# Kernel tuning notes

Hardware: AMD Instinct MI355X
Metric: run time of the kernel (lower is better)

## Reference

```python
import jax, jax.numpy as jnp
import numpy as np

EPS = 1e-8  # torch CosineSimilarity default eps


def setup_inputs() -> dict:
    key = jax.random.key(0)
    k_emb, k_ei, k_w1, k_w2, k_b1, k_b2 = jax.random.split(key, 6)
    N, H, E = 50000, 256, 300000
    emb = jax.random.normal(k_emb, (N, H), dtype=jnp.float32)
    edge_index = jax.random.randint(k_ei, (2, E), 0, N, dtype=jnp.int64)
    # Xavier-uniform init for the two Linear layers (fan_in = fan_out = H)
    limit = float(np.sqrt(6.0 / (H + H)))
    W1 = jax.random.uniform(k_w1, (H, H), minval=-limit, maxval=limit, dtype=jnp.float32)
    W2 = jax.random.uniform(k_w2, (H, H), minval=-limit, maxval=limit, dtype=jnp.float32)
    b1 = jnp.zeros((H,), dtype=jnp.float32)
    b2 = jnp.zeros((H,), dtype=jnp.float32)
    return {"emb": emb, "edge_index": edge_index, "W1": W1, "b1": b1, "W2": W2, "b2": b2}


def _mlp(x, W1, b1, W2, b2):
    # Linear -> Dropout(eval: identity) -> ReLU -> Linear
    h = jax.nn.relu(x @ W1.T + b1)
    return h @ W2.T + b2


def _cosine(a, b):
    # torch.nn.CosineSimilarity(dim=1): dot / (max(||a||, eps) * max(||b||, eps))
    dot = jnp.sum(a * b, axis=1)
    na = jnp.maximum(jnp.linalg.norm(a, axis=1), EPS)
    nb = jnp.maximum(jnp.linalg.norm(b, axis=1), EPS)
    return dot / (na * nb)


def reference(emb, edge_index, W1, b1, W2, b2):
    col, row = edge_index[0], edge_index[1]
    f1 = emb[col]  # [E, H]
    f2 = emb[row]  # [E, H]
    g1 = _mlp(f1, W1, b1, W2, b2)
    g2 = _mlp(f2, W1, b1, W2, b2)
    return _cosine(g1, g2)  # [E] per-edge attention logits
```

## Files before the change

### kernel.cpp

```cpp
#include <hip/hip_runtime.h>
#include <stdint.h>

#define H 256
#define EPS 1e-8f

typedef __bf16 bf16x8 __attribute__((ext_vector_type(8)));
typedef float  f32x4  __attribute__((ext_vector_type(4)));

__device__ __forceinline__ unsigned short f2bf(float f) {
  unsigned u = __builtin_bit_cast(unsigned, f);
  u += 0x7FFFu + ((u >> 16) & 1u);
  return (unsigned short)(u >> 16);
}
__device__ __forceinline__ float bflo(unsigned u){ return __builtin_bit_cast(float, u << 16); }
__device__ __forceinline__ float bfhi(unsigned u){ return __builtin_bit_cast(float, u & 0xFFFF0000u); }

__device__ __forceinline__ void g2l16(const void* g, void* l) {
  __builtin_amdgcn_global_load_lds((__attribute__((address_space(1))) void*)g,
                                   (__attribute__((address_space(3))) void*)l, 16, 0, 0);
}

__global__ __launch_bounds__(256) void conv_bf16_kernel(
    const float* __restrict__ src, unsigned short* __restrict__ dst, int valid, int total) {
  int i = (blockIdx.x * 256 + threadIdx.x) * 4;
  if (i >= total) return;
  float4 v = make_float4(0.f, 0.f, 0.f, 0.f);
  if (i < valid) v = *(const float4*)(src + i);
  ushort4 o;
  o.x = f2bf(v.x); o.y = f2bf(v.y); o.z = f2bf(v.z); o.w = f2bf(v.w);
  *(ushort4*)(dst + i) = o;
}

__global__ __launch_bounds__(256) void conv_w_kernel(
    const float* __restrict__ W1, const float* __restrict__ W2,
    unsigned short* __restrict__ w1B, unsigned short* __restrict__ w2B) {
  int i = (blockIdx.x * 256 + threadIdx.x) * 4;
  const int HH = H * H;
  if (i >= 2 * HH) return;
  const float* s = (i < HH) ? W1 : W2;
  unsigned short* d = (i < HH) ? w1B : w2B;
  int j = (i < HH) ? i : i - HH;
  float4 v = *(const float4*)(s + j);
  ushort4 o;
  o.x = f2bf(v.x); o.y = f2bf(v.y); o.z = f2bf(v.z); o.w = f2bf(v.w);
  *(ushort4*)(d + j) = o;
}

__global__ __launch_bounds__(256) void fused_mlp_kernel(
    const unsigned short* __restrict__ A,
    const unsigned short* __restrict__ W1,
    const unsigned short* __restrict__ W2,
    const float* __restrict__ b1, const float* __restrict__ b2,
    unsigned short* __restrict__ G,
    float* __restrict__ rn) {
  __shared__ unsigned short sA[64 * 32];
  __shared__ unsigned short sW[256 * 32];
  __shared__ unsigned short sW2[256 * 32];
  __shared__ unsigned short sH[64 * 256];
  __shared__ float ssb[64][2];

  const int tid  = threadIdx.x;
  const int wave = tid >> 6, lane = tid & 63;
  const int quad = lane >> 4, l16 = lane & 15;
  const int wr = wave >> 1, wn = wave & 1;
  const size_t bm = blockIdx.x;

  const int arow = tid >> 2, kch = (tid & 3) * 8;
  const unsigned short* gA  = A  + ((bm * 64 + arow) * H + kch);
  const unsigned short* gW1 = W1 + (size_t)arow * H + kch;
  const unsigned short* gW2 = W2 + (size_t)arow * H + kch;
  unsigned short* lA  = sA  + tid * 8;
  unsigned short* lW  = sW  + tid * 8;
  unsigned short* lW2 = sW2 + tid * 8;

  f32x4 acc[8][2];
#pragma unroll
  for (int i = 0; i < 8; i++)
#pragma unroll
    for (int j = 0; j < 2; j++) acc[i][j] = (f32x4){0.f, 0.f, 0.f, 0.f};

#pragma unroll
  for (int ks = 0; ks < 8; ++ks) {
    const int k0 = ks * 32;
    if (ks) __syncthreads();
    g2l16(gA + k0, lA);
#pragma unroll
    for (int c = 0; c < 4; c++)
      g2l16(gW1 + (size_t)(c * 64) * H + k0, lW + c * 2048);
    __syncthreads();

    bf16x8 wf[8], af[2];
#pragma unroll
    for (int i = 0; i < 8; i++)
      wf[i] = *(const bf16x8*)(sW + ((wn * 128 + i * 16 + l16) * 32 + quad * 8));
#pragma unroll
    for (int j = 0; j < 2; j++)
      af[j] = *(const bf16x8*)(sA + ((wr * 32 + j * 16 + l16) * 32 + quad * 8));
#pragma unroll
    for (int i = 0; i < 8; i++)
#pragma unroll
      for (int j = 0; j < 2; j++)
        acc[i][j] = __builtin_amdgcn_mfma_f32_16x16x32_bf16(wf[i], af[j], acc[i][j], 0, 0, 0);
  }

#pragma unroll
  for (int c = 0; c < 4; c++)
    g2l16(gW2 + (size_t)(c * 64) * H, lW2 + c * 2048);

#pragma unroll
  for (int i = 0; i < 8; i++) {
    const int hcol = wn * 128 + i * 16 + quad * 4;
    const float4 bv = *(const float4*)(b1 + hcol);
#pragma unroll
    for (int j = 0; j < 2; j++) {
      const int row = wr * 32 + j * 16 + l16;
      f32x4 v = acc[i][j];
      unsigned short h0 = f2bf(fmaxf(v[0] + bv.x, 0.f));
      unsigned short h1 = f2bf(fmaxf(v[1] + bv.y, 0.f));
      unsigned short h2 = f2bf(fmaxf(v[2] + bv.z, 0.f));
      unsigned short h3 = f2bf(fmaxf(v[3] + bv.w, 0.f));
      uint2 p;
      p.x = (unsigned)h0 | ((unsigned)h1 << 16);
      p.y = (unsigned)h2 | ((unsigned)h3 << 16);
      unsigned off = (unsigned)(row * 512 + hcol * 2) ^ ((unsigned)(row & 7) << 4);
      *(uint2*)((char*)sH + off) = p;
    }
  }

  __syncthreads();

  f32x4 acc2[2][8];
#pragma unroll
  for (int i = 0; i < 2; i++)
#pragma unroll
    for (int j = 0; j < 8; j++) acc2[i][j] = (f32x4){0.f, 0.f, 0.f, 0.f};

#pragma unroll
  for (int ks = 0; ks < 8; ++ks) {
    if (ks) {
      __syncthreads();
#pragma unroll
      for (int c = 0; c < 4; c++)
        g2l16(gW2 + (size_t)(c * 64) * H + ks * 32, lW2 + c * 2048);
      __syncthreads();
    }
    bf16x8 hf[2], wf2[8];
#pragma unroll
    for (int i = 0; i < 2; i++) {
      const int hrow = wr * 32 + i * 16 + l16;
      unsigned off = (unsigned)(hrow * 512 + ks * 64 + quad * 16) ^ ((unsigned)(hrow & 7) << 4);
      hf[i] = *(const bf16x8*)((const char*)sH + off);
    }
#pragma unroll
    for (int j = 0; j < 8; j++)
      wf2[j] = *(const bf16x8*)(sW2 + ((wn * 128 + j * 16 + l16) * 32 + quad * 8));
#pragma unroll
    for (int i = 0; i < 2; i++)
#pragma unroll
      for (int j = 0; j < 8; j++)
        acc2[i][j] = __builtin_amdgcn_mfma_f32_16x16x32_bf16(hf[i], wf2[j], acc2[i][j], 0, 0, 0);
  }

  float b2v[8];
#pragma unroll
  for (int j = 0; j < 8; j++) b2v[j] = b2[wn * 128 + j * 16 + l16];
#pragma unroll
  for (int i = 0; i < 2; i++)
#pragma unroll
    for (int j = 0; j < 8; j++)
#pragma unroll
      for (int r = 0; r < 4; r++) acc2[i][j][r] += b2v[j];

  float ss[2][4];
#pragma unroll
  for (int i = 0; i < 2; i++)
#pragma unroll
    for (int r = 0; r < 4; r++) {
      float s = 0.f;
#pragma unroll
      for (int j = 0; j < 8; j++) s += acc2[i][j][r] * acc2[i][j][r];
      ss[i][r] = s;
    }
#pragma unroll
  for (int m = 1; m < 16; m <<= 1)
#pragma unroll
    for (int i = 0; i < 2; i++)
#pragma unroll
      for (int r = 0; r < 4; r++) ss[i][r] += __shfl_xor(ss[i][r], m, 64);
  if (l16 == 0) {
#pragma unroll
    for (int i = 0; i < 2; i++)
#pragma unroll
      for (int r = 0; r < 4; r++) ssb[wr * 32 + i * 16 + quad * 4 + r][wn] = ss[i][r];
  }
  __syncthreads();
  if (tid < 64) {
    float s2 = ssb[tid][0] + ssb[tid][1];
    rn[bm * 64 + tid] = 1.f / fmaxf(sqrtf(s2), EPS);
  }

#pragma unroll
  for (int i = 0; i < 2; i++)
#pragma unroll
    for (int j = 0; j < 8; j++) {
      const int gcol = wn * 128 + j * 16 + l16;
#pragma unroll
      for (int r = 0; r < 4; r++) {
        const size_t grow = bm * 64 + wr * 32 + i * 16 + quad * 4 + r;
        G[grow * H + gcol] = f2bf(acc2[i][j][r]);
      }
    }
}

__device__ __forceinline__ float dot_u4(uint4 a, uint4 b) {
  float s;
  s  = bflo(a.x) * bflo(b.x) + bfhi(a.x) * bfhi(b.x);
  s += bflo(a.y) * bflo(b.y) + bfhi(a.y) * bfhi(b.y);
  s += bflo(a.z) * bflo(b.z) + bfhi(a.z) * bfhi(b.z);
  s += bflo(a.w) * bflo(b.w) + bfhi(a.w) * bfhi(b.w);
  return s;
}

__global__ __launch_bounds__(256) void edge_cos_kernel(
    const int* __restrict__ ei, const unsigned short* __restrict__ g,
    const float* __restrict__ rn, float* __restrict__ out, int E) {
  const int lane = threadIdx.x & 63;
  const int wid  = threadIdx.x >> 6;
  const int l8   = lane & 7;
  const int sub  = lane >> 3;
  const int e    = blockIdx.x * 32 + wid * 8 + sub;
  if (e >= E) return;
  const int c = ei[e], r = ei[E + e];
  const uint4* gc = (const uint4*)(g + (size_t)c * H);
  const uint4* gr = (const uint4*)(g + (size_t)r * H);
  uint4 a0 = gc[l8], a1 = gc[l8 + 8], a2 = gc[l8 + 16], a3 = gc[l8 + 24];
  uint4 b0 = gr[l8], b1 = gr[l8 + 8], b2 = gr[l8 + 16], b3 = gr[l8 + 24];
  float d = dot_u4(a0, b0) + dot_u4(a1, b1) + dot_u4(a2, b2) + dot_u4(a3, b3);
  d += __shfl_xor(d, 4, 8);
  d += __shfl_xor(d, 2, 8);
  d += __shfl_xor(d, 1, 8);
  if (l8 == 0) out[e] = d * rn[c] * rn[r];
}

extern "C" void kernel_launch(void* const* d_in, const int* in_sizes, int n_in,
                              void* d_out, int out_size, void* d_ws, size_t ws_size,
                              hipStream_t stream) {
  const float* emb = (const float*)d_in[0];
  const int*   ei  = (const int*)d_in[1];
  const float* W1  = (const float*)d_in[2];
  const float* b1  = (const float*)d_in[3];
  const float* W2  = (const float*)d_in[4];
  const float* b2  = (const float*)d_in[5];
  float* out = (float*)d_out;

  const int NH = in_sizes[0];
  const int N  = NH / H;
  const int E  = in_sizes[1] / 2;
  const int Mp = ((N + 63) / 64) * 64;

  char* ws = (char*)d_ws;
  unsigned short* embB = (unsigned short*)ws; ws += (size_t)Mp * H * 2;
  unsigned short* gB   = (unsigned short*)ws; ws += (size_t)Mp * H * 2;
  unsigned short* w1B  = (unsigned short*)ws; ws += (size_t)H * H * 2;
  unsigned short* w2B  = (unsigned short*)ws; ws += (size_t)H * H * 2;
  float* rn            = (float*)ws;

  conv_bf16_kernel<<<(Mp * H / 4 + 255) / 256, 256, 0, stream>>>(emb, embB, NH, Mp * H);
  conv_w_kernel<<<(2 * H * H / 4 + 255) / 256, 256, 0, stream>>>(W1, W2, w1B, w2B);

  fused_mlp_kernel<<<Mp / 64, 256, 0, stream>>>(embB, w1B, w2B, b1, b2, gB, rn);

  edge_cos_kernel<<<(E + 31) / 32, 256, 0, stream>>>(ei, gB, rn, out, E);
}
```

Measured before the change: 165.7 us.

## Fuse embedding bf16 conversion into MLP kernel and double-buffer weight staging

Removes the separate fp32-to-bf16 conversion pass over the embedding table. The MLP kernel now reads fp32 rows directly, keeping three k-tiles in flight in registers and converting them into a double-buffered LDS tile. Weight tiles for both GEMMs are also double-buffered, so each iteration prefetches the next tile with a single barrier instead of two. This saves a full write and re-read of the bf16 embedding copy and a kernel launch, at the cost of more registers and higher LDS pressure per block.

Result: faster. 155.3 us (-6.3%).

```diff
diff --git a/kernel.cpp b/kernel.cpp
--- a/kernel.cpp
+++ b/kernel.cpp
@@ -18,17 +18,6 @@
 __device__ __forceinline__ void g2l16(const void* g, void* l) {
   __builtin_amdgcn_global_load_lds((__attribute__((address_space(1))) void*)g,
                                    (__attribute__((address_space(3))) void*)l, 16, 0, 0);
-}
-
-__global__ __launch_bounds__(256) void conv_bf16_kernel(
-    const float* __restrict__ src, unsigned short* __restrict__ dst, int valid, int total) {
-  int i = (blockIdx.x * 256 + threadIdx.x) * 4;
-  if (i >= total) return;
-  float4 v = make_float4(0.f, 0.f, 0.f, 0.f);
-  if (i < valid) v = *(const float4*)(src + i);
-  ushort4 o;
-  o.x = f2bf(v.x); o.y = f2bf(v.y); o.z = f2bf(v.z); o.w = f2bf(v.w);
-  *(ushort4*)(dst + i) = o;
 }
 
 __global__ __launch_bounds__(256) void conv_w_kernel(
@@ -47,15 +36,14 @@
 }
 
 __global__ __launch_bounds__(256) void fused_mlp_kernel(
-    const unsigned short* __restrict__ A,
+    const float* __restrict__ Af,
     const unsigned short* __restrict__ W1,
     const unsigned short* __restrict__ W2,
     const float* __restrict__ b1, const float* __restrict__ b2,
     unsigned short* __restrict__ G,
-    float* __restrict__ rn) {
-  __shared__ unsigned short sA[64 * 32];
-  __shared__ unsigned short sW[256 * 32];
-  __shared__ unsigned short sW2[256 * 32];
+    float* __restrict__ rn, int N) {
+  __shared__ unsigned short sA[2][64 * 32];
+  __shared__ unsigned short sW[2][256 * 32];
   __shared__ unsigned short sH[64 * 256];
   __shared__ float ssb[64][2];
 
@@ -66,12 +54,38 @@
   const size_t bm = blockIdx.x;
 
   const int arow = tid >> 2, kch = (tid & 3) * 8;
-  const unsigned short* gA  = A  + ((bm * 64 + arow) * H + kch);
+  const int grow = (int)bm * 64 + arow;
+  const bool avalid = grow < N;
+  const float* gAf = Af + (size_t)grow * H + kch;
   const unsigned short* gW1 = W1 + (size_t)arow * H + kch;
   const unsigned short* gW2 = W2 + (size_t)arow * H + kch;
-  unsigned short* lA  = sA  + tid * 8;
-  unsigned short* lW  = sW  + tid * 8;
-  unsigned short* lW2 = sW2 + tid * 8;
+
+  float4 ra[3][2];
+#define LOAD_A(kt, slot)                                                        \
+  do {                                                                          \
+    if (avalid) {                                                               \
+      ra[slot][0] = *(const float4*)(gAf + (kt) * 32);                          \
+      ra[slot][1] = *(const float4*)(gAf + (kt) * 32 + 4);                      \
+    } else {                                                                    \
+      ra[slot][0] = make_float4(0.f, 0.f, 0.f, 0.f);                            \
+      ra[slot][1] = make_float4(0.f, 0.f, 0.f, 0.f);                            \
+    }                                                                           \
+  } while (0)
+#define WRITE_A(buf, slot)                                                      \
+  do {                                                                          \
+    uint4 p;                                                                    \
+    p.x = (unsigned)f2bf(ra[slot][0].x) | ((unsigned)f2bf(ra[slot][0].y) << 16);\
+    p.y = (unsigned)f2bf(ra[slot][0].z) | ((unsigned)f2bf(ra[slot][0].w) << 16);\
+    p.z = (unsigned)f2bf(ra[slot][1].x) | ((unsigned)f2bf(ra[slot][1].y) << 16);\
+    p.w = (unsigned)f2bf(ra[slot][1].z) | ((unsigned)f2bf(ra[slot][1].w) << 16);\
+    *(uint4*)(&sA[buf][tid * 8]) = p;                                           \
+  } while (0)
+#define STAGE_W(gW, kt, buf)                                                    \
+  do {                                                                          \
+    _Pragma("unroll")                                                           \
+    for (int c = 0; c < 4; c++)                                                 \
+      g2l16((gW) + (size_t)(c * 64) * H + (kt) * 32, &sW[buf][c * 2048 + tid * 8]); \
+  } while (0)
 
   f32x4 acc[8][2];
 #pragma unroll
@@ -79,33 +93,34 @@
 #pragma unroll
     for (int j = 0; j < 2; j++) acc[i][j] = (f32x4){0.f, 0.f, 0.f, 0.f};
 
-#pragma unroll
-  for (int ks = 0; ks < 8; ++ks) {
-    const int k0 = ks * 32;
-    if (ks) __syncthreads();
-    g2l16(gA + k0, lA);
-#pragma unroll
-    for (int c = 0; c < 4; c++)
-      g2l16(gW1 + (size_t)(c * 64) * H + k0, lW + c * 2048);
-    __syncthreads();
+  LOAD_A(0, 0); LOAD_A(1, 1); LOAD_A(2, 2);
+  WRITE_A(0, 0);
+  STAGE_W(gW1, 0, 0);
+  __syncthreads();
+
+#pragma unroll
+  for (int kt = 0; kt < 8; ++kt) {
+    if (kt < 5) LOAD_A(kt + 3, (kt + 3) % 3);
+    if (kt < 7) STAGE_W(gW1, kt + 1, (kt + 1) & 1);
+    if (kt == 7) STAGE_W(gW2, 0, 0);
 
     bf16x8 wf[8], af[2];
 #pragma unroll
     for (int i = 0; i < 8; i++)
-      wf[i] = *(const bf16x8*)(sW + ((wn * 128 + i * 16 + l16) * 32 + quad * 8));
+      wf[i] = *(const bf16x8*)(&sW[kt & 1][(wn * 128 + i * 16 + l16) * 32 + quad * 8]);
 #pragma unroll
     for (int j = 0; j < 2; j++)
-      af[j] = *(const bf16x8*)(sA + ((wr * 32 + j * 16 + l16) * 32 + quad * 8));
+      af[j] = *(const bf16x8*)(&sA[kt & 1][(wr * 32 + j * 16 + l16) * 32 + quad * 8]);
+
+    if (kt < 7) WRITE_A((kt + 1) & 1, (kt + 1) % 3);
+
 #pragma unroll
     for (int i = 0; i < 8; i++)
 #pragma unroll
       for (int j = 0; j < 2; j++)
         acc[i][j] = __builtin_amdgcn_mfma_f32_16x16x32_bf16(wf[i], af[j], acc[i][j], 0, 0, 0);
-  }
-
-#pragma unroll
-  for (int c = 0; c < 4; c++)
-    g2l16(gW2 + (size_t)(c * 64) * H, lW2 + c * 2048);
+    __syncthreads();
+  }
 
 #pragma unroll
   for (int i = 0; i < 8; i++) {
@@ -136,29 +151,25 @@
     for (int j = 0; j < 8; j++) acc2[i][j] = (f32x4){0.f, 0.f, 0.f, 0.f};
 
 #pragma unroll
-  for (int ks = 0; ks < 8; ++ks) {
-    if (ks) {
-      __syncthreads();
-#pragma unroll
-      for (int c = 0; c < 4; c++)
-        g2l16(gW2 + (size_t)(c * 64) * H + ks * 32, lW2 + c * 2048);
-      __syncthreads();
-    }
+  for (int kt = 0; kt < 8; ++kt) {
+    if (kt < 7) STAGE_W(gW2, kt + 1, (kt + 1) & 1);
+
     bf16x8 hf[2], wf2[8];
 #pragma unroll
     for (int i = 0; i < 2; i++) {
       const int hrow = wr * 32 + i * 16 + l16;
-      unsigned off = (unsigned)(hrow * 512 + ks * 64 + quad * 16) ^ ((unsigned)(hrow & 7) << 4);
+      unsigned off = (unsigned)(hrow * 512 + kt * 64 + quad * 16) ^ ((unsigned)(hrow & 7) << 4);
       hf[i] = *(const bf16x8*)((const char*)sH + off);
     }
 #pragma unroll
     for (int j = 0; j < 8; j++)
-      wf2[j] = *(const bf16x8*)(sW2 + ((wn * 128 + j * 16 + l16) * 32 + quad * 8));
+      wf2[j] = *(const bf16x8*)(&sW[kt & 1][(wn * 128 + j * 16 + l16) * 32 + quad * 8]);
 #pragma unroll
     for (int i = 0; i < 2; i++)
 #pragma unroll
       for (int j = 0; j < 8; j++)
         acc2[i][j] = __builtin_amdgcn_mfma_f32_16x16x32_bf16(hf[i], wf2[j], acc2[i][j], 0, 0, 0);
+    __syncthreads();
   }
 
   float b2v[8];
@@ -206,10 +217,13 @@
       const int gcol = wn * 128 + j * 16 + l16;
 #pragma unroll
       for (int r = 0; r < 4; r++) {
-        const size_t grow = bm * 64 + wr * 32 + i * 16 + quad * 4 + r;
-        G[grow * H + gcol] = f2bf(acc2[i][j][r]);
+        const size_t grow2 = bm * 64 + wr * 32 + i * 16 + quad * 4 + r;
+        G[grow2 * H + gcol] = f2bf(acc2[i][j][r]);
       }
     }
+#undef LOAD_A
+#undef WRITE_A
+#undef STAGE_W
 }
 
 __device__ __forceinline__ float dot_u4(uint4 a, uint4 b) {
@@ -259,16 +273,14 @@
   const int Mp = ((N + 63) / 64) * 64;
 
   char* ws = (char*)d_ws;
-  unsigned short* embB = (unsigned short*)ws; ws += (size_t)Mp * H * 2;
   unsigned short* gB   = (unsigned short*)ws; ws += (size_t)Mp * H * 2;
   unsigned short* w1B  = (unsigned short*)ws; ws += (size_t)H * H * 2;
   unsigned short* w2B  = (unsigned short*)ws; ws += (size_t)H * H * 2;
   float* rn            = (float*)ws;
 
-  conv_bf16_kernel<<<(Mp * H / 4 + 255) / 256, 256, 0, stream>>>(emb, embB, NH, Mp * H);
   conv_w_kernel<<<(2 * H * H / 4 + 255) / 256, 256, 0, stream>>>(W1, W2, w1B, w2B);
 
-  fused_mlp_kernel<<<Mp / 64, 256, 0, stream>>>(embB, w1B, w2B, b1, b2, gB, rn);
+  fused_mlp_kernel<<<Mp / 64, 256, 0, stream>>>(emb, w1B, w2B, b1, b2, gB, rn, N);
 
   edge_cos_kernel<<<(E + 31) / 32, 256, 0, stream>>>(ei, gB, rn, out, E);
 }
```

## Fuse fp32-to-bf16 embedding conversion into MLP kernel and load operands directly

Applied to the files above, without the earlier changes.

Removes the separate embedding conversion kernel and its bf16 workspace. The MLP kernel now reads fp32 embeddings directly into registers and packs them to bf16. W1 and W2 fragments are loaded straight from global memory (expected to hit L2) instead of being staged through LDS with barriers. This avoids a full write and re-read of the embedding table and drops most syncthreads. In exchange, weight loads are uncoalesced per-wave global reads and register pressure rises.

After: 240.8 us. 1.45x slower.

```diff
diff --git a/kernel.cpp b/kernel.cpp
--- a/kernel.cpp
+++ b/kernel.cpp
@@ -15,20 +15,13 @@
 __device__ __forceinline__ float bflo(unsigned u){ return __builtin_bit_cast(float, u << 16); }
 __device__ __forceinline__ float bfhi(unsigned u){ return __builtin_bit_cast(float, u & 0xFFFF0000u); }
 
-__device__ __forceinline__ void g2l16(const void* g, void* l) {
-  __builtin_amdgcn_global_load_lds((__attribute__((address_space(1))) void*)g,
-                                   (__attribute__((address_space(3))) void*)l, 16, 0, 0);
-}
-
-__global__ __launch_bounds__(256) void conv_bf16_kernel(
-    const float* __restrict__ src, unsigned short* __restrict__ dst, int valid, int total) {
-  int i = (blockIdx.x * 256 + threadIdx.x) * 4;
-  if (i >= total) return;
-  float4 v = make_float4(0.f, 0.f, 0.f, 0.f);
-  if (i < valid) v = *(const float4*)(src + i);
-  ushort4 o;
-  o.x = f2bf(v.x); o.y = f2bf(v.y); o.z = f2bf(v.z); o.w = f2bf(v.w);
-  *(ushort4*)(dst + i) = o;
+__device__ __forceinline__ bf16x8 pack8(float4 a, float4 b) {
+  uint4 p;
+  p.x = (unsigned)f2bf(a.x) | ((unsigned)f2bf(a.y) << 16);
+  p.y = (unsigned)f2bf(a.z) | ((unsigned)f2bf(a.w) << 16);
+  p.z = (unsigned)f2bf(b.x) | ((unsigned)f2bf(b.y) << 16);
+  p.w = (unsigned)f2bf(b.z) | ((unsigned)f2bf(b.w) << 16);
+  return __builtin_bit_cast(bf16x8, p);
 }
 
 __global__ __launch_bounds__(256) void conv_w_kernel(
@@ -47,15 +40,12 @@
 }
 
 __global__ __launch_bounds__(256) void fused_mlp_kernel(
-    const unsigned short* __restrict__ A,
+    const float* __restrict__ Af,
     const unsigned short* __restrict__ W1,
     const unsigned short* __restrict__ W2,
     const float* __restrict__ b1, const float* __restrict__ b2,
     unsigned short* __restrict__ G,
-    float* __restrict__ rn) {
-  __shared__ unsigned short sA[64 * 32];
-  __shared__ unsigned short sW[256 * 32];
-  __shared__ unsigned short sW2[256 * 32];
+    float* __restrict__ rn, int N) {
   __shared__ unsigned short sH[64 * 256];
   __shared__ float ssb[64][2];
 
@@ -65,13 +55,13 @@
   const int wr = wave >> 1, wn = wave & 1;
   const size_t bm = blockIdx.x;
 
-  const int arow = tid >> 2, kch = (tid & 3) * 8;
-  const unsigned short* gA  = A  + ((bm * 64 + arow) * H + kch);
-  const unsigned short* gW1 = W1 + (size_t)arow * H + kch;
-  const unsigned short* gW2 = W2 + (size_t)arow * H + kch;
-  unsigned short* lA  = sA  + tid * 8;
-  unsigned short* lW  = sW  + tid * 8;
-  unsigned short* lW2 = sW2 + tid * 8;
+  const int arow0 = (int)bm * 64 + wr * 32 + l16;
+  const int arow1 = arow0 + 16;
+  const bool v0 = arow0 < N, v1 = arow1 < N;
+  const float* pA0 = Af + (size_t)arow0 * H + quad * 8;
+  const float* pA1 = Af + (size_t)arow1 * H + quad * 8;
+  const unsigned short* pW1 = W1 + (size_t)(wn * 128 + l16) * H + quad * 8;
+  const unsigned short* pW2 = W2 + (size_t)(wn * 128 + l16) * H + quad * 8;
 
   f32x4 acc[8][2];
 #pragma unroll
@@ -79,33 +69,26 @@
 #pragma unroll
     for (int j = 0; j < 2; j++) acc[i][j] = (f32x4){0.f, 0.f, 0.f, 0.f};
 
-#pragma unroll
-  for (int ks = 0; ks < 8; ++ks) {
-    const int k0 = ks * 32;
-    if (ks) __syncthreads();
-    g2l16(gA + k0, lA);
-#pragma unroll
-    for (int c = 0; c < 4; c++)
-      g2l16(gW1 + (size_t)(c * 64) * H + k0, lW + c * 2048);
-    __syncthreads();
-
-    bf16x8 wf[8], af[2];
+  const float4 z4 = make_float4(0.f, 0.f, 0.f, 0.f);
+#pragma unroll
+  for (int kt = 0; kt < 8; ++kt) {
+    const int k0 = kt * 32;
+    bf16x8 wf[8];
 #pragma unroll
     for (int i = 0; i < 8; i++)
-      wf[i] = *(const bf16x8*)(sW + ((wn * 128 + i * 16 + l16) * 32 + quad * 8));
-#pragma unroll
-    for (int j = 0; j < 2; j++)
-      af[j] = *(const bf16x8*)(sA + ((wr * 32 + j * 16 + l16) * 32 + quad * 8));
-#pragma unroll
-    for (int i = 0; i < 8; i++)
-#pragma unroll
-      for (int j = 0; j < 2; j++)
-        acc[i][j] = __builtin_amdgcn_mfma_f32_16x16x32_bf16(wf[i], af[j], acc[i][j], 0, 0, 0);
-  }
-
-#pragma unroll
-  for (int c = 0; c < 4; c++)
-    g2l16(gW2 + (size_t)(c * 64) * H, lW2 + c * 2048);
+      wf[i] = *(const bf16x8*)(pW1 + (size_t)(i * 16) * H + k0);
+    float4 a00 = v0 ? *(const float4*)(pA0 + k0)     : z4;
+    float4 a01 = v0 ? *(const float4*)(pA0 + k0 + 4) : z4;
+    float4 a10 = v1 ? *(const float4*)(pA1 + k0)     : z4;
+    float4 a11 = v1 ? *(const float4*)(pA1 + k0 + 4) : z4;
+    bf16x8 af0 = pack8(a00, a01);
+    bf16x8 af1 = pack8(a10, a11);
+#pragma unroll
+    for (int i = 0; i < 8; i++) {
+      acc[i][0] = __builtin_amdgcn_mfma_f32_16x16x32_bf16(wf[i], af0, acc[i][0], 0, 0, 0);
+      acc[i][1] = __builtin_amdgcn_mfma_f32_16x16x32_bf16(wf[i], af1, acc[i][1], 0, 0, 0);
+    }
+  }
 
 #pragma unroll
   for (int i = 0; i < 8; i++) {
@@ -136,24 +119,18 @@
     for (int j = 0; j < 8; j++) acc2[i][j] = (f32x4){0.f, 0.f, 0.f, 0.f};
 
 #pragma unroll
-  for (int ks = 0; ks < 8; ++ks) {
-    if (ks) {
-      __syncthreads();
-#pragma unroll
-      for (int c = 0; c < 4; c++)
-        g2l16(gW2 + (size_t)(c * 64) * H + ks * 32, lW2 + c * 2048);
-      __syncthreads();
-    }
-    bf16x8 hf[2], wf2[8];
+  for (int kt = 0; kt < 8; ++kt) {
+    bf16x8 wf2[8];
+#pragma unroll
+    for (int j = 0; j < 8; j++)
+      wf2[j] = *(const bf16x8*)(pW2 + (size_t)(j * 16) * H + kt * 32);
+    bf16x8 hf[2];
 #pragma unroll
     for (int i = 0; i < 2; i++) {
       const int hrow = wr * 32 + i * 16 + l16;
-      unsigned off = (unsigned)(hrow * 512 + ks * 64 + quad * 16) ^ ((unsigned)(hrow & 7) << 4);
+      unsigned off = (unsigned)(hrow * 512 + kt * 64 + quad * 16) ^ ((unsigned)(hrow & 7) << 4);
       hf[i] = *(const bf16x8*)((const char*)sH + off);
     }
-#pragma unroll
-    for (int j = 0; j < 8; j++)
-      wf2[j] = *(const bf16x8*)(sW2 + ((wn * 128 + j * 16 + l16) * 32 + quad * 8));
 #pragma unroll
     for (int i = 0; i < 2; i++)
 #pragma unroll
@@ -259,16 +236,14 @@
   const int Mp = ((N + 63) / 64) * 64;
 
   char* ws = (char*)d_ws;
-  unsigned short* embB = (unsigned short*)ws; ws += (size_t)Mp * H * 2;
   unsigned short* gB   = (unsigned short*)ws; ws += (size_t)Mp * H * 2;
   unsigned short* w1B  = (unsigned short*)ws; ws += (size_t)H * H * 2;
   unsigned short* w2B  = (unsigned short*)ws; ws += (size_t)H * H * 2;
   float* rn            = (float*)ws;
 
-  conv_bf16_kernel<<<(Mp * H / 4 + 255) / 256, 256, 0, stream>>>(emb, embB, NH, Mp * H);
   conv_w_kernel<<<(2 * H * H / 4 + 255) / 256, 256, 0, stream>>>(W1, W2, w1B, w2B);
 
-  fused_mlp_kernel<<<Mp / 64, 256, 0, stream>>>(embB, w1B, w2B, b1, b2, gB, rn);
+  fused_mlp_kernel<<<Mp / 64, 256, 0, stream>>>(emb, w1B, w2B, b1, b2, gB, rn, N);
 
   edge_cos_kernel<<<(E + 31) / 32, 256, 0, stream>>>(ei, gB, rn, out, E);
 }
```
